# Kernel optimization log

Measured on AMD Instinct MI355X. Metric: run time of the kernel, lower is better.

Reference implementation:

```python
import jax, jax.numpy as jnp
import numpy as np

NEG_SLOPE = 0.2  # PyG GATConv default negative_slope


def _gat_edge_forward(x, edge_index, edge_attr, W, W_edge, att_src, att_dst, att_edge, bias):
    N = x.shape[0]
    H, C = att_src.shape
    src, dst = edge_index[0], edge_index[1]

    # --- add self loops with edge_attr fill_value='mean' (PyG default) ---
    ones = jnp.ones((edge_attr.shape[0],), dtype=x.dtype)
    cnt = jax.ops.segment_sum(ones, dst, num_segments=N)  # [N]
    attr_sum = jax.ops.segment_sum(edge_attr, dst, num_segments=N)  # [N, edge_dim]
    loop_attr = attr_sum / jnp.maximum(cnt, 1.0)[:, None]  # mean, 0 if no in-edges
    loop_idx = jnp.arange(N, dtype=edge_index.dtype)
    src_all = jnp.concatenate([src, loop_idx])
    dst_all = jnp.concatenate([dst, loop_idx])
    attr_all = jnp.concatenate([edge_attr, loop_attr], axis=0)  # [E+N, edge_dim]

    # --- linear projections ---
    x_l = (x @ W).reshape(N, H, C)  # [N,H,C]; GATConv uses same lin for src/dst
    a_src = jnp.einsum('nhc,hc->nh', x_l, att_src)  # [N,H]
    a_dst = jnp.einsum('nhc,hc->nh', x_l, att_dst)  # [N,H]
    e = (attr_all @ W_edge).reshape(-1, H, C)  # [E+N,H,C]
    a_edge = jnp.einsum('ehc,hc->eh', e, att_edge)  # [E+N,H]

    # --- per-edge attention logits + segment softmax over incoming edges ---
    logits = jax.nn.leaky_relu(a_src[src_all] + a_dst[dst_all] + a_edge, NEG_SLOPE)
    m = jax.ops.segment_max(logits, dst_all, num_segments=N)  # [N,H]
    p = jnp.exp(logits - m[dst_all])
    denom = jax.ops.segment_sum(p, dst_all, num_segments=N)  # [N,H]
    alpha = p / denom[dst_all]  # [E+N,H]

    # --- weighted scatter aggregation ---
    msgs = alpha[:, :, None] * x_l[src_all]  # [E+N,H,C]
    out = jax.ops.segment_sum(msgs, dst_all, num_segments=N)  # [N,H,C]
    return out.reshape(N, H * C) + bias  # concat=True -> [N, H*C]


def setup_inputs() -> dict:
    key = jax.random.key(0)
    ks = jax.random.split(key, 8)
    N, E, DIN, EDIM, H, C = 100000, 1600000, 128, 16, 4, 32
    s = 1.0 / np.sqrt(DIN)
    return {
        'x': jax.random.normal(ks[0], (N, DIN), jnp.float32),
        'edge_index': jax.random.randint(ks[1], (2, E), 0, N, jnp.int64),
        'edge_attr': jax.random.normal(ks[2], (E, EDIM), jnp.float32),
        'W': jax.random.normal(ks[3], (DIN, H * C), jnp.float32) * s,
        'W_edge': jax.random.normal(ks[4], (EDIM, H * C), jnp.float32) * (1.0 / np.sqrt(EDIM)),
        'att_src': jax.random.normal(ks[5], (H, C), jnp.float32) * 0.1,
        'att_dst': jax.random.normal(ks[6], (H, C), jnp.float32) * 0.1,
        'att_edge': jax.random.normal(ks[7], (H, C), jnp.float32) * 0.1,
        'bias': jnp.zeros((H * C,), jnp.float32),
    }


def reference(x, edge_index, edge_attr, W, W_edge, att_src, att_dst, att_edge, bias):
    return _gat_edge_forward(x, edge_index, edge_attr, W, W_edge, att_src, att_dst, att_edge, bias)
```

## Files before the change

### kernel.cpp

```cpp
#include <hip/hip_runtime.h>
#include <hip/hip_fp16.h>
#include <math.h>

#define NEG_SLOPE 0.2f
typedef unsigned short ushort_t;
typedef unsigned int uint_t;

__global__ void k_prep(const int* __restrict__ ei, int* __restrict__ is64,
                       int* __restrict__ deg, int N,
                       const float* __restrict__ W_edge, const float* __restrict__ att_edge,
                       float* __restrict__ v_edge) {
  int b = blockIdx.x, t = threadIdx.x;
  if (b == 0) {
    __shared__ int any;
    if (t == 0) any = 0;
    __syncthreads();
    if (ei[2 * t + 1] != 0) atomicOr(&any, 1);
    __syncthreads();
    if (t == 0) *is64 = (any == 0) ? 1 : 0;
  } else if (b == 1) {
    if (t < 64) {
      int h = t >> 4, j = t & 15;
      float s = 0.f;
#pragma unroll
      for (int c = 0; c < 32; ++c) s += W_edge[j * 128 + h * 32 + c] * att_edge[h * 32 + c];
      v_edge[t] = s;
    }
  } else {
    int i = (b - 2) * 256 + t;
    if (i < N) deg[i] = 0;
  }
}

__global__ __launch_bounds__(256) void k1_xl(
    const float* __restrict__ x, const float* __restrict__ W,
    const float* __restrict__ att_src, const float* __restrict__ att_dst,
    ushort_t* __restrict__ x_l_h, float* __restrict__ a_src, float* __restrict__ a_dst, int N) {
  __shared__ float Wc[32 * 128];
  __shared__ float Xc[32 * 64];
  const int t = threadIdx.x;
  const int tcol = t & 31;
  const int trow = t >> 5;
  const int row0 = blockIdx.x * 64;
  const int r = t & 63, kq = t >> 6;
  const float4 aw_s = *(const float4*)&att_src[tcol * 4];
  const float4 aw_d = *(const float4*)&att_dst[tcol * 4];
  float acc[8][4];
#pragma unroll
  for (int i = 0; i < 8; ++i) { acc[i][0] = acc[i][1] = acc[i][2] = acc[i][3] = 0.f; }

  for (int kc = 0; kc < 4; ++kc) {
    float4 wreg[4];
#pragma unroll
    for (int q = 0; q < 4; ++q) wreg[q] = *(const float4*)&W[kc * 4096 + (q * 256 + t) * 4];
    float xs8[8];
    int grow = row0 + r;
    if (grow < N) {
      *(float4*)&xs8[0] = *(const float4*)&x[grow * 128 + kc * 32 + kq * 8];
      *(float4*)&xs8[4] = *(const float4*)&x[grow * 128 + kc * 32 + kq * 8 + 4];
    } else {
#pragma unroll
      for (int q = 0; q < 8; ++q) xs8[q] = 0.f;
    }
    __syncthreads();
#pragma unroll
    for (int q = 0; q < 4; ++q) *(float4*)&Wc[(q * 256 + t) * 4] = wreg[q];
#pragma unroll
    for (int q = 0; q < 8; ++q) Xc[(kq * 8 + q) * 64 + r] = xs8[q];
    __syncthreads();
#pragma unroll
    for (int kk = 0; kk < 32; ++kk) {
      float4 wv = *(const float4*)&Wc[kk * 128 + tcol * 4];
      float xr[8];
      *(float4*)&xr[0] = *(const float4*)&Xc[kk * 64 + trow * 8];
      *(float4*)&xr[4] = *(const float4*)&Xc[kk * 64 + trow * 8 + 4];
#pragma unroll
      for (int ri = 0; ri < 8; ++ri) {
        acc[ri][0] += xr[ri] * wv.x;
        acc[ri][1] += xr[ri] * wv.y;
        acc[ri][2] += xr[ri] * wv.z;
        acc[ri][3] += xr[ri] * wv.w;
      }
    }
  }
#pragma unroll
  for (int ri = 0; ri < 8; ++ri) {
    int grow = row0 + trow * 8 + ri;
    float asp = acc[ri][0] * aw_s.x + acc[ri][1] * aw_s.y + acc[ri][2] * aw_s.z + acc[ri][3] * aw_s.w;
    float adp = acc[ri][0] * aw_d.x + acc[ri][1] * aw_d.y + acc[ri][2] * aw_d.z + acc[ri][3] * aw_d.w;
#pragma unroll
    for (int m = 1; m < 8; m <<= 1) { asp += __shfl_xor(asp, m); adp += __shfl_xor(adp, m); }
    if (grow < N) {
      __half2 h0 = __floats2half2_rn(acc[ri][0], acc[ri][1]);
      __half2 h1 = __floats2half2_rn(acc[ri][2], acc[ri][3]);
      uint2 u; u.x = *(uint_t*)&h0; u.y = *(uint_t*)&h1;
      *(uint2*)&x_l_h[(size_t)grow * 128 + tcol * 4] = u;
      if ((tcol & 7) == 0) {
        a_src[grow * 4 + (tcol >> 3)] = asp;
        a_dst[grow * 4 + (tcol >> 3)] = adp;
      }
    }
  }
}

__global__ void k_hist(const int* __restrict__ ei, const int* __restrict__ is64,
                       int* __restrict__ deg, int* __restrict__ rank, int E) {
  int i = blockIdx.x * blockDim.x + threadIdx.x;
  if (i >= E) return;
  int dst = (*is64) ? ei[2 * (E + i)] : ei[E + i];
  rank[i] = atomicAdd(&deg[dst], 1);
}

__global__ void k_scan1(const int* __restrict__ deg, int* __restrict__ bsum, int N) {
  __shared__ int lds[256];
  int b = blockIdx.x, t = threadIdx.x;
  int base = b * 1024 + t * 4;
  int s = 0;
  if (base + 3 < N) {
    int4 v = *(const int4*)&deg[base];
    s = v.x + v.y + v.z + v.w;
  } else {
    for (int q = 0; q < 4; ++q) if (base + q < N) s += deg[base + q];
  }
  lds[t] = s; __syncthreads();
  for (int st = 128; st > 0; st >>= 1) {
    if (t < st) lds[t] += lds[t + st];
    __syncthreads();
  }
  if (t == 0) bsum[b] = lds[0];
}

__global__ void k_scan2(const int* __restrict__ bsum, int* __restrict__ boff, int NB) {
  __shared__ int lds[256];
  int t = threadIdx.x;
  int v = (t < NB) ? bsum[t] : 0;
  lds[t] = v;
  __syncthreads();
  for (int st = 1; st < 256; st <<= 1) {
    int add = (t >= st) ? lds[t - st] : 0;
    __syncthreads();
    lds[t] += add;
    __syncthreads();
  }
  if (t < NB) boff[t] = lds[t] - v;
}

__global__ void k_scan3(const int* __restrict__ deg, const int* __restrict__ boff,
                        int* __restrict__ offs, int N) {
  __shared__ int lds[256];
  int b = blockIdx.x, t = threadIdx.x;
  int base = b * 1024 + t * 4;
  int v[4]; int s = 0;
#pragma unroll
  for (int q = 0; q < 4; ++q) { v[q] = (base + q < N) ? deg[base + q] : 0; s += v[q]; }
  lds[t] = s;
  __syncthreads();
  for (int st = 1; st < 256; st <<= 1) {
    int add = (t >= st) ? lds[t - st] : 0;
    __syncthreads();
    lds[t] += add;
    __syncthreads();
  }
  int run = boff[b] + lds[t] - s;
#pragma unroll
  for (int q = 0; q < 4; ++q) {
    if (base + q < N) offs[base + q] = run;
    run += v[q];
  }
}

__global__ __launch_bounds__(256) void k_scatter(
    const int* __restrict__ ei, const int* __restrict__ is64,
    const int* __restrict__ rank, const int* __restrict__ offs,
    const float* __restrict__ edge_attr, const float* __restrict__ v_edge,
    int4* __restrict__ rec, int E) {
  __shared__ float ve[64];
  int t = threadIdx.x;
  if (t < 64) ve[t] = v_edge[t];
  __syncthreads();
  int i = blockIdx.x * 256 + t;
  if (i >= E) return;
  int f = *is64;
  int src = f ? ei[2 * i] : ei[i];
  int dst = f ? ei[2 * (E + i)] : ei[E + i];
  float a16[16];
  *(float4*)&a16[0]  = *(const float4*)&edge_attr[(size_t)i * 16];
  *(float4*)&a16[4]  = *(const float4*)&edge_attr[(size_t)i * 16 + 4];
  *(float4*)&a16[8]  = *(const float4*)&edge_attr[(size_t)i * 16 + 8];
  *(float4*)&a16[12] = *(const float4*)&edge_attr[(size_t)i * 16 + 12];
  float ae[4];
#pragma unroll
  for (int h = 0; h < 4; ++h) {
    float s = 0.f;
#pragma unroll
    for (int j = 0; j < 16; ++j) s += a16[j] * ve[h * 16 + j];
    ae[h] = s;
  }
  int pos = offs[dst] + rank[i];
  __half2 e01 = __floats2half2_rn(ae[0], ae[1]);
  __half2 e23 = __floats2half2_rn(ae[2], ae[3]);
  int4 r; r.x = *(int*)&e01; r.y = *(int*)&e23; r.z = src; r.w = 0;
  rec[pos] = r;
}

__global__ __launch_bounds__(256) void k3_softmax(
    int4* __restrict__ rec, const float* __restrict__ a_src,
    const float* __restrict__ a_dst, const int* __restrict__ deg,
    const int* __restrict__ offs, float* __restrict__ inv_den,
    float* __restrict__ aloop, int N) {
  int t = threadIdx.x;
  int node = blockIdx.x * 16 + (t >> 4);
  int sl = t & 15;
  if (node >= N) return;
  int off = offs[node], dg = deg[node];
  float ad4[4]; *(float4*)ad4 = *(const float4*)&a_dst[(size_t)node * 4];
  uint2* rec8 = (uint2*)rec;
  float den[4] = {0, 0, 0, 0}, sae[4] = {0, 0, 0, 0};
  for (int i = sl; i < dg; i += 16) {
    int pos = off + i;
    int4 u = rec[pos];
    float2 e01 = __half22float2(*(const __half2*)&u.x);
    float2 e23 = __half22float2(*(const __half2*)&u.y);
    float aev[4] = {e01.x, e01.y, e23.x, e23.y};
    int src = u.z;
    float as4[4]; *(float4*)as4 = *(const float4*)&a_src[(size_t)src * 4];
    float p4[4];
#pragma unroll
    for (int h = 0; h < 4; ++h) {
      float lg = as4[h] + ad4[h] + aev[h];
      lg = (lg >= 0.f) ? lg : NEG_SLOPE * lg;
      float pv = __expf(lg);
      p4[h] = pv;
      den[h] += pv;
      sae[h] += aev[h];
    }
    __half2 p01 = __floats2half2_rn(p4[0], p4[1]);
    __half2 p23 = __floats2half2_rn(p4[2], p4[3]);
    uint2 w; w.x = *(uint_t*)&p01; w.y = *(uint_t*)&p23;
    rec8[(size_t)pos * 2] = w;
  }
#pragma unroll
  for (int m = 1; m < 16; m <<= 1) {
#pragma unroll
    for (int h = 0; h < 4; ++h) { den[h] += __shfl_xor(den[h], m); sae[h] += __shfl_xor(sae[h], m); }
  }
  if (sl == 0) {
    float as4[4]; *(float4*)as4 = *(const float4*)&a_src[(size_t)node * 4];
    float inv_cnt = 1.f / (float)(dg > 0 ? dg : 1);
    float id4[4], al4[4];
#pragma unroll
    for (int h = 0; h < 4; ++h) {
      float lae = sae[h] * inv_cnt;
      float lg = as4[h] + ad4[h] + lae;
      lg = (lg >= 0.f) ? lg : NEG_SLOPE * lg;
      float pl = __expf(lg);
      float dt = den[h] + pl;
      float iv = 1.f / dt;
      id4[h] = iv; al4[h] = pl * iv;
    }
    *(float4*)&inv_den[(size_t)node * 4] = *(float4*)id4;
    *(float4*)&aloop[(size_t)node * 4]  = *(float4*)al4;
  }
}

__global__ __launch_bounds__(256) void k4_agg(
    const int4* __restrict__ rec, const ushort_t* __restrict__ x_l_h,
    const float* __restrict__ inv_den, const float* __restrict__ aloop,
    const int* __restrict__ deg, const int* __restrict__ offs,
    const float* __restrict__ bias, float* __restrict__ out, int N) {
  int lane = threadIdx.x & 63;
  int node = blockIdx.x * 4 + (threadIdx.x >> 6);
  if (node >= N) return;
  int off = offs[node], dg = deg[node];
  int h = lane >> 4;
  float iv = inv_den[(size_t)node * 4 + h];
  float al = aloop[(size_t)node * 4 + h];
  const uint_t* xu = (const uint_t*)x_l_h;
  float accx, accy;
  {
    uint_t v = xu[(size_t)node * 64 + lane];
    float2 f = __half22float2(*(const __half2*)&v);
    accx = al * f.x; accy = al * f.y;
  }
  int i = 0;
  for (; i + 4 <= dg; i += 4) {
    int4 u0 = rec[off + i], u1 = rec[off + i + 1], u2 = rec[off + i + 2], u3 = rec[off + i + 3];
    uint_t w0 = (h & 2) ? (uint_t)u0.y : (uint_t)u0.x;
    uint_t w1 = (h & 2) ? (uint_t)u1.y : (uint_t)u1.x;
    uint_t w2 = (h & 2) ? (uint_t)u2.y : (uint_t)u2.x;
    uint_t w3 = (h & 2) ? (uint_t)u3.y : (uint_t)u3.x;
    float2 q0 = __half22float2(*(const __half2*)&w0);
    float2 q1 = __half22float2(*(const __half2*)&w1);
    float2 q2 = __half22float2(*(const __half2*)&w2);
    float2 q3 = __half22float2(*(const __half2*)&w3);
    float a0 = ((h & 1) ? q0.y : q0.x) * iv;
    float a1 = ((h & 1) ? q1.y : q1.x) * iv;
    float a2 = ((h & 1) ? q2.y : q2.x) * iv;
    float a3 = ((h & 1) ? q3.y : q3.x) * iv;
    uint_t v0 = xu[(size_t)u0.z * 64 + lane];
    uint_t v1 = xu[(size_t)u1.z * 64 + lane];
    uint_t v2 = xu[(size_t)u2.z * 64 + lane];
    uint_t v3 = xu[(size_t)u3.z * 64 + lane];
    float2 f0 = __half22float2(*(const __half2*)&v0);
    float2 f1 = __half22float2(*(const __half2*)&v1);
    float2 f2 = __half22float2(*(const __half2*)&v2);
    float2 f3 = __half22float2(*(const __half2*)&v3);
    accx += a0 * f0.x; accy += a0 * f0.y;
    accx += a1 * f1.x; accy += a1 * f1.y;
    accx += a2 * f2.x; accy += a2 * f2.y;
    accx += a3 * f3.x; accy += a3 * f3.y;
  }
  for (; i < dg; ++i) {
    int4 u = rec[off + i];
    uint_t w = (h & 2) ? (uint_t)u.y : (uint_t)u.x;
    float2 q = __half22float2(*(const __half2*)&w);
    float a = ((h & 1) ? q.y : q.x) * iv;
    uint_t v = xu[(size_t)u.z * 64 + lane];
    float2 f = __half22float2(*(const __half2*)&v);
    accx += a * f.x; accy += a * f.y;
  }
  float2 b2 = *(const float2*)&bias[2 * lane];
  float2 o; o.x = accx + b2.x; o.y = accy + b2.y;
  *(float2*)&out[(size_t)node * 128 + 2 * lane] = o;
}

extern "C" void kernel_launch(void* const* d_in, const int* in_sizes, int n_in,
                              void* d_out, int out_size, void* d_ws, size_t ws_size,
                              hipStream_t stream) {
  const float* x        = (const float*)d_in[0];
  const int*   ei       = (const int*)  d_in[1];
  const float* eattr    = (const float*)d_in[2];
  const float* W        = (const float*)d_in[3];
  const float* W_edge   = (const float*)d_in[4];
  const float* att_src  = (const float*)d_in[5];
  const float* att_dst  = (const float*)d_in[6];
  const float* att_edge = (const float*)d_in[7];
  const float* bias     = (const float*)d_in[8];
  float* out = (float*)d_out;
  const int N = in_sizes[0] / 128;
  const int E = in_sizes[1] / 2;
  (void)n_in; (void)out_size; (void)ws_size;

  char* base = (char*)d_ws;
  size_t off = 0;
  auto take = [&](size_t bytes) -> void* {
    void* p = base + off;
    off = (off + bytes + 255) & ~(size_t)255;
    return p;
  };
  ushort_t* x_l_h = (ushort_t*)take((size_t)N * 128 * 2);
  float* a_src    = (float*)take((size_t)N * 4 * 4);
  float* a_dst    = (float*)take((size_t)N * 4 * 4);
  float* v_edge   = (float*)take(64 * 4);
  int4*  rec      = (int4*)take((size_t)E * 16);
  float* inv_den  = (float*)take((size_t)N * 4 * 4);
  float* aloop    = (float*)take((size_t)N * 4 * 4);
  int*   deg      = (int*)take((size_t)N * 4);
  int*   offs     = (int*)take((size_t)N * 4);
  int*   rank     = (int*)take((size_t)E * 4);
  int*   bsum     = (int*)take(256 * 4);
  int*   boff     = (int*)take(256 * 4);
  int*   is64     = (int*)take(4);

  const int NB = (N + 1023) / 1024;

  hipLaunchKernelGGL(k_prep, dim3(2 + (N + 255) / 256), dim3(256), 0, stream,
                     ei, is64, deg, N, W_edge, att_edge, v_edge);
  hipLaunchKernelGGL(k1_xl, dim3((N + 63) / 64), dim3(256), 0, stream,
                     x, W, att_src, att_dst, x_l_h, a_src, a_dst, N);
  hipLaunchKernelGGL(k_hist, dim3((E + 255) / 256), dim3(256), 0, stream, ei, is64, deg, rank, E);
  hipLaunchKernelGGL(k_scan1, dim3(NB), dim3(256), 0, stream, deg, bsum, N);
  hipLaunchKernelGGL(k_scan2, dim3(1), dim3(256), 0, stream, bsum, boff, NB);
  hipLaunchKernelGGL(k_scan3, dim3(NB), dim3(256), 0, stream, deg, boff, offs, N);
  hipLaunchKernelGGL(k_scatter, dim3((E + 255) / 256), dim3(256), 0, stream,
                     ei, is64, rank, offs, eattr, v_edge, rec, E);
  hipLaunchKernelGGL(k3_softmax, dim3((N + 15) / 16), dim3(256), 0, stream,
                     rec, a_src, a_dst, deg, offs, inv_den, aloop, N);
  hipLaunchKernelGGL(k4_agg, dim3((N + 3) / 4), dim3(256), 0, stream,
                     rec, x_l_h, inv_den, aloop, deg, offs, bias, out, N);
}
```

Baseline: 300.7 us.

## Fuse softmax into aggregation and merge histogram into projection kernel

```diff
diff --git a/kernel.cpp b/kernel.cpp
--- a/kernel.cpp
+++ b/kernel.cpp
@@ -32,12 +32,22 @@
   }
 }
 
-__global__ __launch_bounds__(256) void k1_xl(
+__global__ __launch_bounds__(256) void k1_hist(
     const float* __restrict__ x, const float* __restrict__ W,
     const float* __restrict__ att_src, const float* __restrict__ att_dst,
-    ushort_t* __restrict__ x_l_h, float* __restrict__ a_src, float* __restrict__ a_dst, int N) {
+    ushort_t* __restrict__ x_l_h, float* __restrict__ a_src, float* __restrict__ a_dst, int N,
+    const int* __restrict__ ei, const int* __restrict__ is64,
+    int* __restrict__ deg, int* __restrict__ rank, int E, int nb1) {
   __shared__ float Wc[32 * 128];
   __shared__ float Xc[32 * 64];
+  if (blockIdx.x >= nb1) {
+    int i = (blockIdx.x - nb1) * 256 + threadIdx.x;
+    if (i < E) {
+      int dst = (*is64) ? ei[2 * (E + i)] : ei[E + i];
+      rank[i] = atomicAdd(&deg[dst], 1);
+    }
+    return;
+  }
   const int t = threadIdx.x;
   const int tcol = t & 31;
   const int trow = t >> 5;
@@ -101,14 +111,6 @@
       }
     }
   }
-}
-
-__global__ void k_hist(const int* __restrict__ ei, const int* __restrict__ is64,
-                       int* __restrict__ deg, int* __restrict__ rank, int E) {
-  int i = blockIdx.x * blockDim.x + threadIdx.x;
-  if (i >= E) return;
-  int dst = (*is64) ? ei[2 * (E + i)] : ei[E + i];
-  rank[i] = atomicAdd(&deg[dst], 1);
 }
 
 __global__ void k_scan1(const int* __restrict__ deg, int* __restrict__ bsum, int N) {
@@ -203,69 +205,9 @@
   rec[pos] = r;
 }
 
-__global__ __launch_bounds__(256) void k3_softmax(
-    int4* __restrict__ rec, const float* __restrict__ a_src,
-    const float* __restrict__ a_dst, const int* __restrict__ deg,
-    const int* __restrict__ offs, float* __restrict__ inv_den,
-    float* __restrict__ aloop, int N) {
-  int t = threadIdx.x;
-  int node = blockIdx.x * 16 + (t >> 4);
-  int sl = t & 15;
-  if (node >= N) return;
-  int off = offs[node], dg = deg[node];
-  float ad4[4]; *(float4*)ad4 = *(const float4*)&a_dst[(size_t)node * 4];
-  uint2* rec8 = (uint2*)rec;
-  float den[4] = {0, 0, 0, 0}, sae[4] = {0, 0, 0, 0};
-  for (int i = sl; i < dg; i += 16) {
-    int pos = off + i;
-    int4 u = rec[pos];
-    float2 e01 = __half22float2(*(const __half2*)&u.x);
-    float2 e23 = __half22float2(*(const __half2*)&u.y);
-    float aev[4] = {e01.x, e01.y, e23.x, e23.y};
-    int src = u.z;
-    float as4[4]; *(float4*)as4 = *(const float4*)&a_src[(size_t)src * 4];
-    float p4[4];
-#pragma unroll
-    for (int h = 0; h < 4; ++h) {
-      float lg = as4[h] + ad4[h] + aev[h];
-      lg = (lg >= 0.f) ? lg : NEG_SLOPE * lg;
-      float pv = __expf(lg);
-      p4[h] = pv;
-      den[h] += pv;
-      sae[h] += aev[h];
-    }
-    __half2 p01 = __floats2half2_rn(p4[0], p4[1]);
-    __half2 p23 = __floats2half2_rn(p4[2], p4[3]);
-    uint2 w; w.x = *(uint_t*)&p01; w.y = *(uint_t*)&p23;
-    rec8[(size_t)pos * 2] = w;
-  }
-#pragma unroll
-  for (int m = 1; m < 16; m <<= 1) {
-#pragma unroll
-    for (int h = 0; h < 4; ++h) { den[h] += __shfl_xor(den[h], m); sae[h] += __shfl_xor(sae[h], m); }
-  }
-  if (sl == 0) {
-    float as4[4]; *(float4*)as4 = *(const float4*)&a_src[(size_t)node * 4];
-    float inv_cnt = 1.f / (float)(dg > 0 ? dg : 1);
-    float id4[4], al4[4];
-#pragma unroll
-    for (int h = 0; h < 4; ++h) {
-      float lae = sae[h] * inv_cnt;
-      float lg = as4[h] + ad4[h] + lae;
-      lg = (lg >= 0.f) ? lg : NEG_SLOPE * lg;
-      float pl = __expf(lg);
-      float dt = den[h] + pl;
-      float iv = 1.f / dt;
-      id4[h] = iv; al4[h] = pl * iv;
-    }
-    *(float4*)&inv_den[(size_t)node * 4] = *(float4*)id4;
-    *(float4*)&aloop[(size_t)node * 4]  = *(float4*)al4;
-  }
-}
-
-__global__ __launch_bounds__(256) void k4_agg(
+__global__ __launch_bounds__(256) void k34_agg(
     const int4* __restrict__ rec, const ushort_t* __restrict__ x_l_h,
-    const float* __restrict__ inv_den, const float* __restrict__ aloop,
+    const float* __restrict__ a_src, const float* __restrict__ a_dst,
     const int* __restrict__ deg, const int* __restrict__ offs,
     const float* __restrict__ bias, float* __restrict__ out, int N) {
   int lane = threadIdx.x & 63;
@@ -273,18 +215,20 @@
   if (node >= N) return;
   int off = offs[node], dg = deg[node];
   int h = lane >> 4;
-  float iv = inv_den[(size_t)node * 4 + h];
-  float al = aloop[(size_t)node * 4 + h];
+  float ad = a_dst[(size_t)node * 4 + h];
   const uint_t* xu = (const uint_t*)x_l_h;
-  float accx, accy;
-  {
-    uint_t v = xu[(size_t)node * 64 + lane];
-    float2 f = __half22float2(*(const __half2*)&v);
-    accx = al * f.x; accy = al * f.y;
-  }
+  float accx = 0.f, accy = 0.f, den = 0.f, sae = 0.f;
   int i = 0;
   for (; i + 4 <= dg; i += 4) {
     int4 u0 = rec[off + i], u1 = rec[off + i + 1], u2 = rec[off + i + 2], u3 = rec[off + i + 3];
+    uint_t v0 = xu[(size_t)u0.z * 64 + lane];
+    uint_t v1 = xu[(size_t)u1.z * 64 + lane];
+    uint_t v2 = xu[(size_t)u2.z * 64 + lane];
+    uint_t v3 = xu[(size_t)u3.z * 64 + lane];
+    float s0 = a_src[(size_t)u0.z * 4 + h];
+    float s1 = a_src[(size_t)u1.z * 4 + h];
+    float s2 = a_src[(size_t)u2.z * 4 + h];
+    float s3 = a_src[(size_t)u3.z * 4 + h];
     uint_t w0 = (h & 2) ? (uint_t)u0.y : (uint_t)u0.x;
     uint_t w1 = (h & 2) ? (uint_t)u1.y : (uint_t)u1.x;
     uint_t w2 = (h & 2) ? (uint_t)u2.y : (uint_t)u2.x;
@@ -293,34 +237,51 @@
     float2 q1 = __half22float2(*(const __half2*)&w1);
     float2 q2 = __half22float2(*(const __half2*)&w2);
     float2 q3 = __half22float2(*(const __half2*)&w3);
-    float a0 = ((h & 1) ? q0.y : q0.x) * iv;
-    float a1 = ((h & 1) ? q1.y : q1.x) * iv;
-    float a2 = ((h & 1) ? q2.y : q2.x) * iv;
-    float a3 = ((h & 1) ? q3.y : q3.x) * iv;
-    uint_t v0 = xu[(size_t)u0.z * 64 + lane];
-    uint_t v1 = xu[(size_t)u1.z * 64 + lane];
-    uint_t v2 = xu[(size_t)u2.z * 64 + lane];
-    uint_t v3 = xu[(size_t)u3.z * 64 + lane];
+    float e0 = (h & 1) ? q0.y : q0.x;
+    float e1 = (h & 1) ? q1.y : q1.x;
+    float e2 = (h & 1) ? q2.y : q2.x;
+    float e3 = (h & 1) ? q3.y : q3.x;
+    float g0 = s0 + ad + e0; g0 = (g0 >= 0.f) ? g0 : NEG_SLOPE * g0;
+    float g1 = s1 + ad + e1; g1 = (g1 >= 0.f) ? g1 : NEG_SLOPE * g1;
+    float g2 = s2 + ad + e2; g2 = (g2 >= 0.f) ? g2 : NEG_SLOPE * g2;
+    float g3 = s3 + ad + e3; g3 = (g3 >= 0.f) ? g3 : NEG_SLOPE * g3;
+    float p0 = __expf(g0), p1 = __expf(g1), p2 = __expf(g2), p3 = __expf(g3);
+    den += p0 + p1 + p2 + p3;
+    sae += e0 + e1 + e2 + e3;
     float2 f0 = __half22float2(*(const __half2*)&v0);
     float2 f1 = __half22float2(*(const __half2*)&v1);
     float2 f2 = __half22float2(*(const __half2*)&v2);
     float2 f3 = __half22float2(*(const __half2*)&v3);
-    accx += a0 * f0.x; accy += a0 * f0.y;
-    accx += a1 * f1.x; accy += a1 * f1.y;
-    accx += a2 * f2.x; accy += a2 * f2.y;
-    accx += a3 * f3.x; accy += a3 * f3.y;
+    accx += p0 * f0.x; accy += p0 * f0.y;
+    accx += p1 * f1.x; accy += p1 * f1.y;
+    accx += p2 * f2.x; accy += p2 * f2.y;
+    accx += p3 * f3.x; accy += p3 * f3.y;
   }
   for (; i < dg; ++i) {
     int4 u = rec[off + i];
+    uint_t v = xu[(size_t)u.z * 64 + lane];
+    float as = a_src[(size_t)u.z * 4 + h];
     uint_t w = (h & 2) ? (uint_t)u.y : (uint_t)u.x;
     float2 q = __half22float2(*(const __half2*)&w);
-    float a = ((h & 1) ? q.y : q.x) * iv;
-    uint_t v = xu[(size_t)u.z * 64 + lane];
+    float ae = (h & 1) ? q.y : q.x;
+    float g = as + ad + ae; g = (g >= 0.f) ? g : NEG_SLOPE * g;
+    float p = __expf(g);
+    den += p; sae += ae;
     float2 f = __half22float2(*(const __half2*)&v);
-    accx += a * f.x; accy += a * f.y;
-  }
+    accx += p * f.x; accy += p * f.y;
+  }
+  float as_n = a_src[(size_t)node * 4 + h];
+  float inv_cnt = 1.f / (float)(dg > 0 ? dg : 1);
+  float gl = as_n + ad + sae * inv_cnt;
+  gl = (gl >= 0.f) ? gl : NEG_SLOPE * gl;
+  float pl = __expf(gl);
+  float iv = 1.f / (den + pl);
+  uint_t vn = xu[(size_t)node * 64 + lane];
+  float2 fn = __half22float2(*(const __half2*)&vn);
   float2 b2 = *(const float2*)&bias[2 * lane];
-  float2 o; o.x = accx + b2.x; o.y = accy + b2.y;
+  float2 o;
+  o.x = (accx + pl * fn.x) * iv + b2.x;
+  o.y = (accy + pl * fn.y) * iv + b2.y;
   *(float2*)&out[(size_t)node * 128 + 2 * lane] = o;
 }
 
@@ -353,8 +314,6 @@
   float* a_dst    = (float*)take((size_t)N * 4 * 4);
   float* v_edge   = (float*)take(64 * 4);
   int4*  rec      = (int4*)take((size_t)E * 16);
-  float* inv_den  = (float*)take((size_t)N * 4 * 4);
-  float* aloop    = (float*)take((size_t)N * 4 * 4);
   int*   deg      = (int*)take((size_t)N * 4);
   int*   offs     = (int*)take((size_t)N * 4);
   int*   rank     = (int*)take((size_t)E * 4);
@@ -363,19 +322,19 @@
   int*   is64     = (int*)take(4);
 
   const int NB = (N + 1023) / 1024;
+  const int nb1 = (N + 63) / 64;
+  const int nbh = (E + 255) / 256;
 
   hipLaunchKernelGGL(k_prep, dim3(2 + (N + 255) / 256), dim3(256), 0, stream,
                      ei, is64, deg, N, W_edge, att_edge, v_edge);
-  hipLaunchKernelGGL(k1_xl, dim3((N + 63) / 64), dim3(256), 0, stream,
-                     x, W, att_src, att_dst, x_l_h, a_src, a_dst, N);
-  hipLaunchKernelGGL(k_hist, dim3((E + 255) / 256), dim3(256), 0, stream, ei, is64, deg, rank, E);
+  hipLaunchKernelGGL(k1_hist, dim3(nb1 + nbh), dim3(256), 0, stream,
+                     x, W, att_src, att_dst, x_l_h, a_src, a_dst, N,
+                     ei, is64, deg, rank, E, nb1);
   hipLaunchKernelGGL(k_scan1, dim3(NB), dim3(256), 0, stream, deg, bsum, N);
   hipLaunchKernelGGL(k_scan2, dim3(1), dim3(256), 0, stream, bsum, boff, NB);
   hipLaunchKernelGGL(k_scan3, dim3(NB), dim3(256), 0, stream, deg, boff, offs, N);
-  hipLaunchKernelGGL(k_scatter, dim3((E + 255) / 256), dim3(256), 0, stream,
+  hipLaunchKernelGGL(k_scatter, dim3(nbh), dim3(256), 0, stream,
                      ei, is64, rank, offs, eattr, v_edge, rec, E);
-  hipLaunchKernelGGL(k3_softmax, dim3((N + 15) / 16), dim3(256), 0, stream,
-                     rec, a_src, a_dst, deg, offs, inv_den, aloop, N);
-  hipLaunchKernelGGL(k4_agg, dim3((N + 3) / 4), dim3(256), 0, stream,
-                     rec, x_l_h, inv_den, aloop, deg, offs, bias, out, N);
-}
+  hipLaunchKernelGGL(k34_agg, dim3((N + 3) / 4), dim3(256), 0, stream,
+                     rec, x_l_h, a_src, a_dst, deg, offs, bias, out, N);
+}
```

New measurement: 268.6 us. 1.12x faster.
